# Optimization experiments

Hardware: AMD Instinct MI355X
Metric: run time of the kernel (lower is better)

The kernel has to match this reference:

```python
import jax, jax.numpy as jnp
import numpy as np

K_NN = 5
COS_EPS = 1e-8  # torch cosine_similarity eps


def setup_inputs() -> dict:
    key = jax.random.key(0)
    ks = jax.random.split(key, 10)
    N1, N2, D, E, H = 2000, 2000, 63, 64, 8
    return {
        "lm_X": jax.random.normal(ks[0], (N1, D), jnp.float32),
        "lm_Y": jax.random.normal(ks[1], (N1, 2), jnp.float32),
        "tg_X": jax.random.normal(ks[2], (N2, D), jnp.float32),
        "tg_Y": jax.random.normal(ks[3], (N2, 2), jnp.float32),
        "lm_delay": jax.random.uniform(ks[4], (N1,), jnp.float32),
        "tg_delay": jax.random.uniform(ks[5], (N2,), jnp.float32),
        # learned params: embedding Linear(input_dim=D+1 -> E) and per-head score weights
        "W_emb": jax.random.normal(ks[6], (E, D + 1), jnp.float32) / np.sqrt(D + 1),
        "b_emb": jnp.zeros((E,), jnp.float32),
        "w1": jax.random.normal(ks[7], (E, H), jnp.float32),
        "w2": jax.random.normal(ks[8], (E, H), jnp.float32),
    }


def _knn_adj(X, k):
    # binary row-wise k-nearest-neighbour adjacency, self excluded
    n = X.shape[0]
    sq = jnp.sum(X * X, axis=1)
    d2 = sq[:, None] + sq[None, :] - 2.0 * (X @ X.T)  # [n, n] squared distances
    d2 = jnp.where(jnp.eye(n, dtype=bool), jnp.inf, d2)  # exclude self
    _, idx = jax.lax.top_k(-d2, k)  # k smallest distances -> [n, k]
    rows = jnp.arange(n)[:, None]
    return jnp.zeros((n, n), X.dtype).at[rows, idx].set(1.0)


def reference(lm_X, lm_Y, tg_X, tg_Y, lm_delay, tg_delay, W_emb, b_emb, w1, w2):
    N1 = lm_X.shape[0]
    N2 = tg_X.shape[0]
    N = N1 + N2
    k = K_NN

    # ---- community-KNN adjacency over landmarks, label aggregation ----
    adj_lm = _knn_adj(lm_X, k)                      # [N1, N1] binary, k ones per row
    y_pred = (adj_lm @ lm_Y) * (1.0 / k)            # [N1, 2]

    # ---- teacher adjacency: (1 - I) with lm block = adj_lm, tg block = 0 ----
    adj_teacher = 1.0 - jnp.eye(N, dtype=lm_X.dtype)
    adj_teacher = adj_teacher.at[:N1, :N1].set(adj_lm)
    adj_teacher = adj_teacher.at[N1:, N1:].set(0.0)

    # ---- node features + embedding ----
    lm_feat = jnp.concatenate([lm_X, lm_delay[:, None]], axis=1)  # [N1, D+1]
    tg_feat = jnp.concatenate([tg_X, tg_delay[:, None]], axis=1)  # [N2, D+1]
    feats = jnp.concatenate([lm_feat, tg_feat], axis=0)           # [N, D+1]
    e = feats @ W_emb.T + b_emb                                    # [N, E]

    # ---- multi-head cosine-similarity edge probabilities (all heads at once) ----
    a = e[:, None, :] * w1.T[None, :, :]            # [N, H, E] : e * w1[:, h]
    b = e[:, None, :] * w2.T[None, :, :]            # [N, H, E] : e * w2[:, h]
    na = jnp.linalg.norm(a, axis=-1)                # [N, H]
    nb = jnp.linalg.norm(b, axis=-1)                # [N, H]
    dot = jnp.einsum("nhe,mhe->nmh", a, b)          # [N, N, H]
    sim = dot / jnp.maximum(na[:, None, :] * nb[None, :, :], COS_EPS)
    alpha = jax.nn.sigmoid(sim)                      # [N, N, H]
    adj = jnp.mean(alpha, axis=-1)                   # [N, N]

    return (y_pred, adj, adj_teacher)
```

## Files before the change

### kernel.cpp

```cpp
#include <hip/hip_runtime.h>
#include <math.h>

#define N1 2000
#define N2 2000
#define NT 4000
#define D  63
#define E  64
#define H  8
#define KNN 5
#define NPAD 4032
#define MPAD 4096

typedef short bf16x8 __attribute__((ext_vector_type(8)));
typedef float f32x4  __attribute__((ext_vector_type(4)));

__device__ __forceinline__ unsigned short f2bf(float x) {
    unsigned u = __float_as_uint(x);
    u = (u + 0x7fffu + ((u >> 16) & 1u)) >> 16;
    return (unsigned short)u;
}

__global__ void k_sq(const float* __restrict__ X, float* __restrict__ sq) {
    int i = blockIdx.x * blockDim.x + threadIdx.x;
    if (i < N1) {
        float s = 0.f;
        for (int d = 0; d < D; ++d) { float v = X[i * D + d]; s += v * v; }
        sq[i] = s;
    }
}

__global__ __launch_bounds__(256) void k_d2(const float* __restrict__ X,
                                            const float* __restrict__ sq,
                                            float* __restrict__ d2) {
    __shared__ float Xi[64][68];
    __shared__ float Xj[64][68];
    int i0 = blockIdx.y * 64, j0 = blockIdx.x * 64;
    int tid = threadIdx.x;
    for (int t = tid; t < 64 * 64; t += 256) {
        int r = t >> 6, c = t & 63;
        int gi = min(i0 + r, N1 - 1);
        int gj = min(j0 + r, N1 - 1);
        Xi[r][c] = (c < D) ? X[gi * D + c] : 0.f;
        Xj[r][c] = (c < D) ? X[gj * D + c] : 0.f;
    }
    __syncthreads();
    int tx = tid & 15, ty = tid >> 4;
    float acc[4][4];
    #pragma unroll
    for (int a = 0; a < 4; ++a)
        #pragma unroll
        for (int b = 0; b < 4; ++b) acc[a][b] = 0.f;

    #pragma unroll 4
    for (int kk = 0; kk < 16; ++kk) {
        float4 av[4], bv[4];
        #pragma unroll
        for (int ii = 0; ii < 4; ++ii) av[ii] = *(const float4*)&Xi[ty + 16 * ii][4 * kk];
        #pragma unroll
        for (int jj = 0; jj < 4; ++jj) bv[jj] = *(const float4*)&Xj[tx + 16 * jj][4 * kk];
        #pragma unroll
        for (int ii = 0; ii < 4; ++ii)
            #pragma unroll
            for (int jj = 0; jj < 4; ++jj)
                acc[ii][jj] += av[ii].x * bv[jj].x + av[ii].y * bv[jj].y +
                               av[ii].z * bv[jj].z + av[ii].w * bv[jj].w;
    }

    #pragma unroll
    for (int ii = 0; ii < 4; ++ii) {
        int i = i0 + ty + 16 * ii;
        #pragma unroll
        for (int jj = 0; jj < 4; ++jj) {
            int j = j0 + tx + 16 * jj;
            if (i < N1 && j < N1) {
                float v = sq[i] + sq[j] - 2.f * acc[ii][jj];
                if (i == j) v = __builtin_inff();
                d2[i * N1 + j] = v;
            }
        }
    }
}

__device__ __forceinline__ bool dless(float d1, int i1, float d2v, int i2) {
    return d1 < d2v || (d1 == d2v && i1 < i2);
}

__device__ __forceinline__ void ins5(float bd[KNN], int bi[KNN], float d, int j) {
    if (dless(d, j, bd[KNN - 1], bi[KNN - 1])) {
        bd[KNN - 1] = d; bi[KNN - 1] = j;
        #pragma unroll
        for (int s = KNN - 1; s > 0; --s) {
            if (dless(bd[s], bi[s], bd[s - 1], bi[s - 1])) {
                float td = bd[s]; bd[s] = bd[s - 1]; bd[s - 1] = td;
                int ti = bi[s]; bi[s] = bi[s - 1]; bi[s - 1] = ti;
            }
        }
    }
}

__global__ __launch_bounds__(256) void k_top5(const float* __restrict__ d2,
                                              const float* __restrict__ lmY,
                                              float* __restrict__ ypred,
                                              int* __restrict__ idx) {
    __shared__ float sd[4 * KNN];
    __shared__ int   si[4 * KNN];
    int i = blockIdx.x;
    int tid = threadIdx.x;
    const float* row = d2 + i * N1;

    float bd[KNN]; int bi[KNN];
    #pragma unroll
    for (int s = 0; s < KNN; ++s) { bd[s] = __builtin_inff(); bi[s] = 0x7fffffff; }
    #pragma unroll
    for (int k = 0; k < 8; ++k) {
        int j = tid + k * 256;
        if (j < N1) ins5(bd, bi, row[j], j);
    }

    int lane = tid & 63, wave = tid >> 6;
    float wd[KNN]; int wi[KNN];
    #pragma unroll
    for (int s = 0; s < KNN; ++s) {
        float d = bd[0]; int ix = bi[0];
        #pragma unroll
        for (int m = 1; m < 64; m <<= 1) {
            float od = __shfl_xor(d, m, 64);
            int   oi = __shfl_xor(ix, m, 64);
            if (dless(od, oi, d, ix)) { d = od; ix = oi; }
        }
        wd[s] = d; wi[s] = ix;
        if (d == bd[0] && ix == bi[0]) {
            #pragma unroll
            for (int q = 0; q < KNN - 1; ++q) { bd[q] = bd[q + 1]; bi[q] = bi[q + 1]; }
            bd[KNN - 1] = __builtin_inff(); bi[KNN - 1] = 0x7fffffff;
        }
    }
    if (lane == 0) {
        #pragma unroll
        for (int s = 0; s < KNN; ++s) { sd[wave * KNN + s] = wd[s]; si[wave * KNN + s] = wi[s]; }
    }
    __syncthreads();
    if (wave == 0) {
        float d = (lane < 4 * KNN) ? sd[lane] : __builtin_inff();
        int  ix = (lane < 4 * KNN) ? si[lane] : 0x7fffffff;
        float rd[KNN]; int ri[KNN];
        #pragma unroll
        for (int s = 0; s < KNN; ++s) {
            float md = d; int mi = ix;
            #pragma unroll
            for (int m = 1; m < 64; m <<= 1) {
                float od = __shfl_xor(md, m, 64);
                int   oi = __shfl_xor(mi, m, 64);
                if (dless(od, oi, md, mi)) { md = od; mi = oi; }
            }
            rd[s] = md; ri[s] = mi;
            if (md == d && mi == ix) { d = __builtin_inff(); ix = 0x7fffffff; }
        }
        if (lane == 0) {
            float y0 = 0.f, y1 = 0.f;
            #pragma unroll
            for (int s = 0; s < KNN; ++s) {
                int j = ri[s];
                y0 += lmY[j * 2];
                y1 += lmY[j * 2 + 1];
                idx[i * KNN + s] = j;
            }
            ypred[i * 2]     = y0 * 0.2f;
            ypred[i * 2 + 1] = y1 * 0.2f;
        }
    }
}

__global__ void k_fillT(float* __restrict__ adjT) {
    int t = blockIdx.x * blockDim.x + threadIdx.x;
    if (t < NT * NT / 4) {
        int r = (t * 4) / NT;
        int c = (t * 4) % NT;
        float v = ((r < N1) != (c < N1)) ? 1.f : 0.f;
        float4 o = {v, v, v, v};
        ((float4*)adjT)[t] = o;
    }
}

__global__ void k_scatter(const int* __restrict__ idx, float* __restrict__ adjT) {
    int t = blockIdx.x * blockDim.x + threadIdx.x;
    if (t < N1 * KNN) {
        int i = t / KNN;
        adjT[i * NT + idx[t]] = 1.f;
    }
}

__global__ __launch_bounds__(64) void k_prep(const float* __restrict__ lmX,
                                             const float* __restrict__ tgX,
                                             const float* __restrict__ lmD,
                                             const float* __restrict__ tgD,
                                             const float* __restrict__ W,
                                             const float* __restrict__ bias,
                                             const float* __restrict__ w1,
                                             const float* __restrict__ w2,
                                             unsigned short* __restrict__ AL,
                                             unsigned short* __restrict__ Bbuf,
                                             float* __restrict__ sB) {
    __shared__ float f[E];
    __shared__ float Wl[E][68];
    int n = blockIdx.x;
    int t = threadIdx.x;
    #pragma unroll
    for (int k = 0; k < 16; ++k) {
        int g = k * 64 + t;
        float4 v = ((const float4*)W)[g];
        int r = g >> 4, c = (g & 15) * 4;
        *(float4*)&Wl[r][c] = v;
    }
    if (t < D)  f[t] = (n < N1) ? lmX[n * D + t] : tgX[(n - N1) * D + t];
    if (t == D) f[t] = (n < N1) ? lmD[n] : tgD[n - N1];
    __syncthreads();
    float s0 = 0.f, s1 = 0.f, s2 = 0.f, s3 = 0.f;
    #pragma unroll
    for (int k = 0; k < 16; ++k) {
        float4 wv = *(const float4*)&Wl[t][4 * k];
        float4 fv = *(const float4*)&f[4 * k];
        s0 += fv.x * wv.x; s1 += fv.y * wv.y; s2 += fv.z * wv.z; s3 += fv.w * wv.w;
    }
    const float en = bias[t] + (s0 + s1) + (s2 + s3);
    Bbuf[n * E + t] = f2bf(en);

    int kc = t >> 5, kq = (t >> 3) & 3, j = t & 7;
    int lane = kq * 16 + (n & 15);
    int nb = n >> 4;
    #pragma unroll
    for (int h = 0; h < H; ++h) {
        float a = en * w1[t * H + h];
        float b = en * w2[t * H + h];
        float na2 = a * a, nb2 = b * b;
        #pragma unroll
        for (int m = 32; m >= 1; m >>= 1) {
            na2 += __shfl_xor(na2, m, 64);
            nb2 += __shfl_xor(nb2, m, 64);
        }
        float val = a * w2[t * H + h] * rsqrtf(na2);
        AL[(((nb * 8 + h) << 1) + kc) * 512 + lane * 8 + j] = f2bf(val);
        if (t == h) sB[n * H + h] = rsqrtf(nb2);
    }
}

__global__ __launch_bounds__(256) void k_adjm(const unsigned short* __restrict__ AL,
                                              const unsigned short* __restrict__ Bbuf,
                                              const float* __restrict__ sB,
                                              float* __restrict__ adj) {
    __shared__ unsigned short Bt[256][68];
    int tid = threadIdx.x;
    int m0 = blockIdx.x * 256, n0 = blockIdx.y * 64;

    #pragma unroll
    for (int it = 0; it < 8; ++it) {
        int g = it * 256 + tid;
        int row = g >> 3, c = g & 7;
        *(bf16x8*)&Bt[row][c * 8] = *(const bf16x8*)&Bbuf[(m0 + row) * E + c * 8];
    }

    int wave = tid >> 6, lane = tid & 63;
    int l15 = lane & 15, kq = lane >> 4;
    int nb = blockIdx.y * 4 + wave;

    bf16x8 afr[H][2];
    #pragma unroll
    for (int h = 0; h < H; ++h)
        #pragma unroll
        for (int kc = 0; kc < 2; ++kc)
            afr[h][kc] = *(const bf16x8*)&AL[(((nb * 8 + h) << 1) + kc) * 512 + lane * 8];

    __syncthreads();

    int nebase = n0 + wave * 16 + kq * 4;

    #pragma unroll 2
    for (int mt = 0; mt < 16; ++mt) {
        int mrow = mt * 16 + l15;
        int mcol = m0 + mrow;
        bf16x8 b0 = *(const bf16x8*)&Bt[mrow][kq * 8];
        bf16x8 b1 = *(const bf16x8*)&Bt[mrow][32 + kq * 8];

        float sbv[H];
        *(f32x4*)&sbv[0] = *(const f32x4*)&sB[mcol * H + 0];
        *(f32x4*)&sbv[4] = *(const f32x4*)&sB[mcol * H + 4];

        f32x4 acc[H];
        #pragma unroll
        for (int h = 0; h < H; ++h) {
            acc[h] = (f32x4){0.f, 0.f, 0.f, 0.f};
            acc[h] = __builtin_amdgcn_mfma_f32_16x16x32_bf16(afr[h][0], b0, acc[h], 0, 0, 0);
            acc[h] = __builtin_amdgcn_mfma_f32_16x16x32_bf16(afr[h][1], b1, acc[h], 0, 0, 0);
        }

        bool mok = (mcol < NT);
        #pragma unroll
        for (int reg = 0; reg < 4; ++reg) {
            int ne = nebase + reg;
            float sum = 0.f;
            #pragma unroll
            for (int h = 0; h < H; ++h) {
                float x = acc[h][reg] * sbv[h];
                float u = x * x;
                float p = fmaf(u, 1.8919e-3f, -2.0833333e-2f);
                p = fmaf(u, p, 0.25f);
                sum = fmaf(x, p, sum);
            }
            if (mok && ne < NT) adj[ne * NT + mcol] = fmaf(sum, 0.125f, 0.5f);
        }
    }
}

extern "C" void kernel_launch(void* const* d_in, const int* in_sizes, int n_in,
                              void* d_out, int out_size, void* d_ws, size_t ws_size,
                              hipStream_t stream) {
    const float* lmX  = (const float*)d_in[0];
    const float* lmY  = (const float*)d_in[1];
    const float* tgX  = (const float*)d_in[2];
    const float* lmD  = (const float*)d_in[4];
    const float* tgD  = (const float*)d_in[5];
    const float* Wemb = (const float*)d_in[6];
    const float* bemb = (const float*)d_in[7];
    const float* w1   = (const float*)d_in[8];
    const float* w2   = (const float*)d_in[9];

    float* out   = (float*)d_out;
    float* ypred = out;
    float* adj   = out + 4000;
    float* adjT  = out + 4000 + 16000000;

    char* ws  = (char*)d_ws;
    float* sq = (float*)ws;
    int*   idx = (int*)(ws + 8000);

    float* d2 = adj;

    char* tz = (char*)adjT;
    unsigned short* AL   = (unsigned short*)tz;
    unsigned short* Bbuf = (unsigned short*)(tz + 4128768);
    float*          sB   = (float*)(tz + 4128768 + 524288);

    k_sq<<<(N1 + 255) / 256, 256, 0, stream>>>(lmX, sq);
    dim3 g2((N1 + 63) / 64, (N1 + 63) / 64);
    k_d2<<<g2, 256, 0, stream>>>(lmX, sq, d2);
    k_top5<<<N1, 256, 0, stream>>>(d2, lmY, ypred, idx);
    k_prep<<<NT, 64, 0, stream>>>(lmX, tgX, lmD, tgD, Wemb, bemb, w1, w2,
                                  AL, Bbuf, sB);
    dim3 ga(MPAD / 256, NPAD / 64);
    k_adjm<<<ga, 256, 0, stream>>>(AL, Bbuf, sB, adj);
    k_fillT<<<(NT * NT / 4 + 255) / 256, 256, 0, stream>>>(adjT);
    k_scatter<<<(N1 * KNN + 255) / 256, 256, 0, stream>>>(idx, adjT);
}
```

Baseline: 236.7 us.

## Fuse teacher-adjacency fill and scatter into adj kernel; batch prep rows

The teacher adjacency fill and KNN scatter are folded into the tail of the adj MFMA kernel, so each block writes its own tile of adjT, and two kernel launches go away. Scratch buffers move from the adjT output region to the workspace, so adjT can be written in the same kernel. k_prep now handles four rows per 256-thread block, which cuts the number of per-block W loads. The cost is extra write traffic and a sync inside the adj kernel. The scatter depends on ordering within the same block after the fill.

```diff
diff --git a/kernel.cpp b/kernel.cpp
--- a/kernel.cpp
+++ b/kernel.cpp
@@ -171,62 +171,44 @@
     }
 }
 
-__global__ void k_fillT(float* __restrict__ adjT) {
-    int t = blockIdx.x * blockDim.x + threadIdx.x;
-    if (t < NT * NT / 4) {
-        int r = (t * 4) / NT;
-        int c = (t * 4) % NT;
-        float v = ((r < N1) != (c < N1)) ? 1.f : 0.f;
-        float4 o = {v, v, v, v};
-        ((float4*)adjT)[t] = o;
-    }
-}
-
-__global__ void k_scatter(const int* __restrict__ idx, float* __restrict__ adjT) {
-    int t = blockIdx.x * blockDim.x + threadIdx.x;
-    if (t < N1 * KNN) {
-        int i = t / KNN;
-        adjT[i * NT + idx[t]] = 1.f;
-    }
-}
-
-__global__ __launch_bounds__(64) void k_prep(const float* __restrict__ lmX,
-                                             const float* __restrict__ tgX,
-                                             const float* __restrict__ lmD,
-                                             const float* __restrict__ tgD,
-                                             const float* __restrict__ W,
-                                             const float* __restrict__ bias,
-                                             const float* __restrict__ w1,
-                                             const float* __restrict__ w2,
-                                             unsigned short* __restrict__ AL,
-                                             unsigned short* __restrict__ Bbuf,
-                                             float* __restrict__ sB) {
-    __shared__ float f[E];
+__global__ __launch_bounds__(256) void k_prep(const float* __restrict__ lmX,
+                                              const float* __restrict__ tgX,
+                                              const float* __restrict__ lmD,
+                                              const float* __restrict__ tgD,
+                                              const float* __restrict__ W,
+                                              const float* __restrict__ bias,
+                                              const float* __restrict__ w1,
+                                              const float* __restrict__ w2,
+                                              unsigned short* __restrict__ AL,
+                                              unsigned short* __restrict__ Bbuf,
+                                              float* __restrict__ sB) {
+    __shared__ float f[4][E];
     __shared__ float Wl[E][68];
-    int n = blockIdx.x;
-    int t = threadIdx.x;
-    #pragma unroll
-    for (int k = 0; k < 16; ++k) {
-        int g = k * 64 + t;
+    int tid = threadIdx.x, lane = tid & 63, wave = tid >> 6;
+    int n = blockIdx.x * 4 + wave;
+    #pragma unroll
+    for (int k = 0; k < 4; ++k) {
+        int g = k * 256 + tid;
         float4 v = ((const float4*)W)[g];
         int r = g >> 4, c = (g & 15) * 4;
         *(float4*)&Wl[r][c] = v;
     }
-    if (t < D)  f[t] = (n < N1) ? lmX[n * D + t] : tgX[(n - N1) * D + t];
-    if (t == D) f[t] = (n < N1) ? lmD[n] : tgD[n - N1];
+    int t = lane;
+    if (t < D)  f[wave][t] = (n < N1) ? lmX[n * D + t] : tgX[(n - N1) * D + t];
+    if (t == D) f[wave][t] = (n < N1) ? lmD[n] : tgD[n - N1];
     __syncthreads();
     float s0 = 0.f, s1 = 0.f, s2 = 0.f, s3 = 0.f;
     #pragma unroll
     for (int k = 0; k < 16; ++k) {
         float4 wv = *(const float4*)&Wl[t][4 * k];
-        float4 fv = *(const float4*)&f[4 * k];
+        float4 fv = *(const float4*)&f[wave][4 * k];
         s0 += fv.x * wv.x; s1 += fv.y * wv.y; s2 += fv.z * wv.z; s3 += fv.w * wv.w;
     }
     const float en = bias[t] + (s0 + s1) + (s2 + s3);
     Bbuf[n * E + t] = f2bf(en);
 
     int kc = t >> 5, kq = (t >> 3) & 3, j = t & 7;
-    int lane = kq * 16 + (n & 15);
+    int alane = kq * 16 + (n & 15);
     int nb = n >> 4;
     #pragma unroll
     for (int h = 0; h < H; ++h) {
@@ -239,7 +221,7 @@
             nb2 += __shfl_xor(nb2, m, 64);
         }
         float val = a * w2[t * H + h] * rsqrtf(na2);
-        AL[(((nb * 8 + h) << 1) + kc) * 512 + lane * 8 + j] = f2bf(val);
+        AL[(((nb * 8 + h) << 1) + kc) * 512 + alane * 8 + j] = f2bf(val);
         if (t == h) sB[n * H + h] = rsqrtf(nb2);
     }
 }
@@ -247,7 +229,9 @@
 __global__ __launch_bounds__(256) void k_adjm(const unsigned short* __restrict__ AL,
                                               const unsigned short* __restrict__ Bbuf,
                                               const float* __restrict__ sB,
-                                              float* __restrict__ adj) {
+                                              const int* __restrict__ idx,
+                                              float* __restrict__ adj,
+                                              float* __restrict__ adjT) {
     __shared__ unsigned short Bt[256][68];
     int tid = threadIdx.x;
     int m0 = blockIdx.x * 256, n0 = blockIdx.y * 64;
@@ -307,6 +291,28 @@
                 sum = fmaf(x, p, sum);
             }
             if (mok && ne < NT) adj[ne * NT + mcol] = fmaf(sum, 0.125f, 0.5f);
+        }
+    }
+
+    #pragma unroll
+    for (int it = 0; it < 16; ++it) {
+        int g = it * 256 + tid;
+        int r = g >> 6;
+        int col = m0 + (g & 63) * 4;
+        int row = n0 + r;
+        if (row < NT && col < NT) {
+            float v = ((row < N1) != (col < N1)) ? 1.f : 0.f;
+            float4 o = {v, v, v, v};
+            *(float4*)&adjT[row * NT + col] = o;
+        }
+    }
+    __syncthreads();
+    for (int p = tid; p < 64 * KNN; p += 256) {
+        int r = p / KNN, s = p - r * KNN;
+        int row = n0 + r;
+        if (row < N1) {
+            int jx = idx[row * KNN + s];
+            if (jx >= m0 && jx < m0 + 256) adjT[row * NT + jx] = 1.f;
         }
     }
 }
@@ -329,25 +335,21 @@
     float* adj   = out + 4000;
     float* adjT  = out + 4000 + 16000000;
 
-    char* ws  = (char*)d_ws;
-    float* sq = (float*)ws;
-    int*   idx = (int*)(ws + 8000);
+    char* ws = (char*)d_ws;
+    unsigned short* AL   = (unsigned short*)ws;
+    unsigned short* Bbuf = (unsigned short*)(ws + 4128768);
+    float*          sB   = (float*)(ws + 4128768 + 524288);
+    float*          sq   = (float*)(ws + 4784128);
+    int*            idx  = (int*)  (ws + 4792128);
 
     float* d2 = adj;
-
-    char* tz = (char*)adjT;
-    unsigned short* AL   = (unsigned short*)tz;
-    unsigned short* Bbuf = (unsigned short*)(tz + 4128768);
-    float*          sB   = (float*)(tz + 4128768 + 524288);
 
     k_sq<<<(N1 + 255) / 256, 256, 0, stream>>>(lmX, sq);
     dim3 g2((N1 + 63) / 64, (N1 + 63) / 64);
     k_d2<<<g2, 256, 0, stream>>>(lmX, sq, d2);
     k_top5<<<N1, 256, 0, stream>>>(d2, lmY, ypred, idx);
-    k_prep<<<NT, 64, 0, stream>>>(lmX, tgX, lmD, tgD, Wemb, bemb, w1, w2,
-                                  AL, Bbuf, sB);
+    k_prep<<<NT / 4, 256, 0, stream>>>(lmX, tgX, lmD, tgD, Wemb, bemb, w1, w2,
+                                       AL, Bbuf, sB);
     dim3 ga(MPAD / 256, NPAD / 64);
-    k_adjm<<<ga, 256, 0, stream>>>(AL, Bbuf, sB, adj);
-    k_fillT<<<(NT * NT / 4 + 255) / 256, 256, 0, stream>>>(adjT);
-    k_scatter<<<(N1 * KNN + 255) / 256, 256, 0, stream>>>(idx, adjT);
-}
+    k_adjm<<<ga, 256, 0, stream>>>(AL, Bbuf, sB, idx, adj, adjT);
+}
```

Measured after the change: 226.0 us. 4.5% less time.
